# Optimization experiments

Hardware: AMD Instinct MI355X
Metric: run time of the kernel (lower is better)

## Reference

```python
import jax, jax.numpy as jnp
import numpy as np

NUM_EXPERTS = 8
HIDDEN = 2048
EXPERT_DIM = 4096
R = 64
LORA_ALPHA = 16
SCALING = LORA_ALPHA / R
TOKENS_PER_EXPERT = 1024


def setup_inputs() -> dict:
    key = jax.random.key(0)
    ks = jax.random.split(key, 7)
    s = lambda shape: 1.0 / np.sqrt(shape[-1])
    return {
        "hidden_states": jax.random.normal(ks[0], (NUM_EXPERTS * TOKENS_PER_EXPERT, HIDDEN), jnp.float32),
        "W_gu": jax.random.normal(ks[1], (2 * EXPERT_DIM, HIDDEN), jnp.float32) * s((HIDDEN,)),
        "A_gu": jax.random.normal(ks[2], (R, HIDDEN), jnp.float32) * s((HIDDEN,)),
        "B_gu": jax.random.normal(ks[3], (2 * EXPERT_DIM, R), jnp.float32) * 0.01,
        "W_d": jax.random.normal(ks[4], (HIDDEN, EXPERT_DIM), jnp.float32) * s((EXPERT_DIM,)),
        "A_d": jax.random.normal(ks[5], (R, EXPERT_DIM), jnp.float32) * s((EXPERT_DIM,)),
        "B_d": jax.random.normal(ks[6], (HIDDEN, R), jnp.float32) * 0.01,
    }


def _lora_linear(x, W, A, B):
    # y = x @ W^T + scaling * (x @ A^T) @ B^T   (nn.Linear convention, no dropout)
    return x @ W.T + (x @ A.T) @ B.T * SCALING


def reference(hidden_states, W_gu, A_gu, B_gu, W_d, A_d, B_d):
    # (E, N, H)
    x = hidden_states.reshape(NUM_EXPERTS, -1, HIDDEN)
    gate_up = _lora_linear(x, W_gu, A_gu, B_gu)          # (E, N, 2*D)
    gate, up = jnp.split(gate_up, 2, axis=-1)             # each (E, N, D)
    h = up * jax.nn.silu(gate)                            # SwiGLU
    out = _lora_linear(h, W_d, A_d, B_d)                  # (E, N, H)
    return out.reshape(-1, HIDDEN)
```

## Files before the change

### kernel.cpp

```cpp
#include <hip/hip_runtime.h>
#include <stdint.h>

typedef __bf16 bf16_t;
typedef __bf16 bf16x8 __attribute__((ext_vector_type(8)));
typedef __bf16 bf16x4 __attribute__((ext_vector_type(4)));
typedef float f32x4 __attribute__((ext_vector_type(4)));

#define GLOAD16(gp, lp)                                                        \
    __builtin_amdgcn_global_load_lds(                                          \
        (const __attribute__((address_space(1))) void*)(gp),                   \
        (__attribute__((address_space(3))) void*)(lp), 16, 0, 0)

#define MFMA16(a, b, c) __builtin_amdgcn_mfma_f32_16x16x32_bf16(a, b, c, 0, 0, 0)

#define SB() __builtin_amdgcn_sched_barrier(0)
#define BAR() asm volatile("s_barrier" ::: "memory")
#define LGKM0() asm volatile("s_waitcnt lgkmcnt(0)" ::: "memory")
#define VMW(n) asm volatile("s_waitcnt vmcnt(" #n ")" ::: "memory")

#define PHASE(GATE, STAGE, PF, MM)                                             \
    do {                                                                       \
        GATE;                                                                  \
        STAGE;                                                                 \
        SB();                                                                  \
        BAR();                                                                 \
        LGKM0();                                                               \
        SB();                                                                  \
        __builtin_amdgcn_s_setprio(1);                                         \
        PF;                                                                    \
        SB();                                                                  \
        MM;                                                                    \
        __builtin_amdgcn_s_setprio(0);                                         \
        SB();                                                                  \
        BAR();                                                                 \
    } while (0)

#define MMCL(aa, bb, mo, no)                                                   \
    do {                                                                       \
        _Pragma("unroll") for (int m_ = 0; m_ < 4; ++m_) {                     \
            _Pragma("unroll") for (int n_ = 0; n_ < 2; ++n_) {                 \
                acc[mo + m_][no + n_] =                                        \
                    MFMA16(aa[m_][0], bb[n_][0], acc[mo + m_][no + n_]);       \
                acc[mo + m_][no + n_] =                                        \
                    MFMA16(aa[m_][1], bb[n_][1], acc[mo + m_][no + n_]);       \
            }                                                                  \
        }                                                                      \
    } while (0)

#define PFA(dst, base, ro)                                                     \
    do {                                                                       \
        _Pragma("unroll") for (int m_ = 0; m_ < 4; ++m_) {                     \
            dst[m_][0] = *(const bf16x8*)((base) + offA0 + (ro + m_) * 1024);  \
            dst[m_][1] = *(const bf16x8*)((base) + offA1 + (ro + m_) * 1024);  \
        }                                                                      \
    } while (0)
#define PFB(dst, base, no)                                                     \
    do {                                                                       \
        _Pragma("unroll") for (int n_ = 0; n_ < 2; ++n_) {                     \
            dst[n_][0] = *(const bf16x8*)((base) + offB0 + (no + n_) * 1024);  \
            dst[n_][1] = *(const bf16x8*)((base) + offB1 + (no + n_) * 1024);  \
        }                                                                      \
    } while (0)


__global__ __launch_bounds__(256) void cvt_all_kernel(
    const float* __restrict__ x, const float* __restrict__ Wgu,
    const float* __restrict__ Bgu, const float* __restrict__ Wd,
    const float* __restrict__ Bd, const float* __restrict__ Agu,
    const float* __restrict__ Ad, bf16_t* __restrict__ X1,
    bf16_t* __restrict__ W1, bf16_t* __restrict__ W2,
    bf16_t* __restrict__ Abf, bf16_t* __restrict__ Adbf) {
    int b = blockIdx.x;
    const float* src;
    bf16_t* dst;
    int cshift, cmask, ldd, coff, lb;
    if (b < 16384) {
        src = x; dst = X1; cshift = 11; cmask = 2047; ldd = 2112; coff = 0; lb = b;
    } else if (b < 32768) {
        src = Wgu; dst = W1; cshift = 11; cmask = 2047; ldd = 2112; coff = 0; lb = b - 16384;
    } else if (b < 33280) {
        src = Bgu; dst = W1; cshift = 6; cmask = 63; ldd = 2112; coff = 2048; lb = b - 32768;
    } else if (b < 41472) {
        src = Wd; dst = W2; cshift = 12; cmask = 4095; ldd = 4160; coff = 0; lb = b - 33280;
    } else if (b < 41600) {
        src = Bd; dst = W2; cshift = 6; cmask = 63; ldd = 4160; coff = 4096; lb = b - 41472;
    } else if (b < 41728) {
        src = Agu; dst = Abf; cshift = 11; cmask = 2047; ldd = 2048; coff = 0; lb = b - 41600;
    } else {
        src = Ad; dst = Adbf; cshift = 12; cmask = 4095; ldd = 4096; coff = 0; lb = b - 41728;
    }
    int idx = (lb * 256 + threadIdx.x) << 2;
    int r = idx >> cshift;
    int c = idx & cmask;
    float4 v = *(const float4*)(src + idx);
    bf16x4 o = {(bf16_t)v.x, (bf16_t)v.y, (bf16_t)v.z, (bf16_t)v.w};
    *(bf16x4*)(dst + (size_t)r * ldd + coff + c) = o;
}

__global__ __launch_bounds__(256) void lora_kernel(const bf16_t* __restrict__ A,
                                                   int lda,
                                                   const bf16_t* __restrict__ Bw,
                                                   int K, bf16_t* __restrict__ dst,
                                                   int ldd, int coff) {
    __shared__ __align__(16) bf16_t As[64 * 64];
    __shared__ __align__(16) bf16_t Bs[64 * 64];
    const int t = threadIdx.x;
    const int m0 = blockIdx.x * 64;
    const int lane = t & 63, w = t >> 6;
    const int ln15 = lane & 15, q = lane >> 4;

    const int lrow = t >> 3;
    const int lchunk = (t & 7) ^ (lrow & 7);
    const bf16_t* gaL = A + (size_t)(m0 + lrow) * lda + lchunk * 8;
    const bf16_t* gbL = Bw + (size_t)lrow * K + lchunk * 8;
    bf16_t* lA = As + t * 8;
    bf16_t* lB = Bs + t * 8;

    const f32x4 z = {0.f, 0.f, 0.f, 0.f};
    f32x4 acc[4];
#pragma unroll
    for (int j = 0; j < 4; ++j) acc[j] = z;

    int aoffs[2], boffs[2][4];
#pragma unroll
    for (int s = 0; s < 2; ++s) {
        int rowa = w * 16 + ln15;
        aoffs[s] = rowa * 64 + (((q + 4 * s) ^ (rowa & 7)) << 3);
#pragma unroll
        for (int j = 0; j < 4; ++j) {
            int rowb = j * 16 + ln15;
            boffs[s][j] = rowb * 64 + (((q + 4 * s) ^ (rowb & 7)) << 3);
        }
    }

    for (int kt = 0; kt < K; kt += 64) {
        GLOAD16(gaL, lA);
        GLOAD16(gaL + (size_t)32 * lda, lA + 32 * 64);
        GLOAD16(gbL, lB);
        GLOAD16(gbL + (size_t)32 * K, lB + 32 * 64);
        __syncthreads();
#pragma unroll
        for (int s = 0; s < 2; ++s) {
            bf16x8 av = *(const bf16x8*)(As + aoffs[s]);
#pragma unroll
            for (int j = 0; j < 4; ++j) {
                bf16x8 bv = *(const bf16x8*)(Bs + boffs[s][j]);
                acc[j] = MFMA16(av, bv, acc[j]);
            }
        }
        __syncthreads();
        gaL += 64;
        gbL += 64;
    }

#pragma unroll
    for (int j = 0; j < 4; ++j)
#pragma unroll
        for (int rg = 0; rg < 4; ++rg) {
            int m = m0 + w * 16 + q * 4 + rg;
            dst[(size_t)m * ldd + coff + j * 16 + ln15] = (bf16_t)(acc[j][rg] * 0.25f);
        }
}

template <int LDA_, int LDB_, int NT_>
__device__ __forceinline__ void gemm8p_core(const bf16_t* __restrict__ gA,
                                            const bf16_t* __restrict__ gB0,
                                            const bf16_t* __restrict__ gB2,
                                            bf16_t* smem, const int t,
                                            const int offA0, const int offA1,
                                            const int offB0, const int offB1,
                                            f32x4 (&acc)[8][4]) {
    static_assert(NT_ & 1, "NT_ must be odd (pairs + tail tile)");
    bf16_t* const As0 = smem;
    bf16_t* const As1 = smem + 16384;
    bf16_t* const Bs0 = smem + 32768;
    bf16_t* const Bs1 = smem + 49152;

    auto stgA0 = [&](int kt, bf16_t* d) {
        GLOAD16(gA + kt, d + t * 8);
        GLOAD16(gA + (size_t)128 * LDA_ + kt, d + 128 * 64 + t * 8);
    };
    auto stgA1 = [&](int kt, bf16_t* d) {
        GLOAD16(gA + (size_t)64 * LDA_ + kt, d + 64 * 64 + t * 8);
        GLOAD16(gA + (size_t)192 * LDA_ + kt, d + 192 * 64 + t * 8);
    };
    auto stgBlo = [&](int kt, bf16_t* d) {
        GLOAD16(gB0 + kt, d + t * 8);
        GLOAD16(gB0 + (size_t)64 * LDB_ + kt, d + 64 * 64 + t * 8);
    };
    auto stgBhi = [&](int kt, bf16_t* d) {
        GLOAD16(gB2 + kt, d + 128 * 64 + t * 8);
        GLOAD16(gB2 + (size_t)64 * LDB_ + kt, d + 192 * 64 + t * 8);
    };

    bf16x8 a0[4][2], a1[4][2], b0e[2][2], b0o[2][2], b1v[2][2];

    stgA0(0, As0);
    stgA1(0, As0);
    stgBlo(0, Bs0);
    stgBhi(0, Bs0);
    stgA0(64, As1);
    stgBlo(64, Bs1);
    stgBhi(64, Bs1);
    VMW(6);
    BAR();
    PFA(a0, As0, 0);
    PFB(b0e, Bs0, 0);

    for (int g = 0; g + 2 < NT_; g += 2) {
        const int k1 = (g + 1) << 6, k2 = (g + 2) << 6, k3 = (g + 3) << 6;
        const bool s3 = (g + 3 < NT_);

        PHASE((void)0, stgA1(k1, As1), PFB(b1v, Bs0, 2), MMCL(a0, b0e, 0, 0));
        PHASE((void)0, stgA0(k2, As0), PFA(a1, As0, 4), MMCL(a0, b1v, 0, 2));
        PHASE(VMW(4), stgBlo(k2, Bs0), PFB(b0o, Bs1, 0), MMCL(a1, b1v, 4, 2));
        PHASE((void)0, stgBhi(k2, Bs0), PFA(a0, As1, 0), MMCL(a1, b0e, 4, 0));
        PHASE((void)0, stgA1(k2, As0), PFB(b1v, Bs1, 2), MMCL(a0, b0o, 0, 0));
        PHASE(VMW(8), if (s3) stgA0(k3, As1), PFA(a1, As1, 4),
              MMCL(a0, b1v, 0, 2));
        PHASE(VMW(2), if (s3) stgBlo(k3, Bs1), PFB(b0e, Bs0, 0),
              MMCL(a1, b1v, 4, 2));
        PHASE((void)0, if (s3) stgBhi(k3, Bs1), PFA(a0, As0, 0),
              MMCL(a1, b0o, 4, 0));
    }

    PHASE((void)0, (void)0, PFB(b1v, Bs0, 2), MMCL(a0, b0e, 0, 0));
    PHASE(VMW(0), (void)0, PFA(a1, As0, 4), MMCL(a0, b1v, 0, 2));
    PHASE((void)0, (void)0, (void)0, MMCL(a1, b1v, 4, 2));
    PHASE((void)0, (void)0, (void)0, MMCL(a1, b0e, 4, 0));
}

__device__ __forceinline__ int eswz(int row, int col) {
    return col ^ (((row >> 2) & 1) << 4) ^ (((row >> 3) & 3) << 2);
}

__global__ __launch_bounds__(512, 2) void gemm1_8p_kernel(
    const bf16_t* __restrict__ X, const bf16_t* __restrict__ Wc,
    bf16_t* __restrict__ X2) {
    __shared__ __align__(16) bf16_t smem[65536];
    const int t = threadIdx.x;
    const int lane = t & 63, wid = t >> 6;
    const int wr = wid >> 2, wc = wid & 3;
    const int ln15 = lane & 15, q = lane >> 4;
    const int n0 = blockIdx.x * 128;
    const int m0 = blockIdx.y * 256;

    const int sw = ln15 & 7;
    const int offA0 = (wr * 128 + ln15) * 64 + ((q ^ sw) << 3);
    const int offA1 = (wr * 128 + ln15) * 64 + (((q + 4) ^ sw) << 3);
    const int offB0 = (wc * 64 + ln15) * 64 + ((q ^ sw) << 3);
    const int offB1 = (wc * 64 + ln15) * 64 + (((q + 4) ^ sw) << 3);

    const int rr = t >> 3;
    const int lch = (t & 7) ^ (rr & 7);
    const bf16_t* gA = X + (size_t)(m0 + rr) * 2112 + lch * 8;
    const bf16_t* gB0 = Wc + (size_t)(n0 + rr) * 2112 + lch * 8;
    const bf16_t* gB2 = Wc + (size_t)(4096 + n0 + rr) * 2112 + lch * 8;

    f32x4 acc[8][4];
    const f32x4 z = {0.f, 0.f, 0.f, 0.f};
#pragma unroll
    for (int i = 0; i < 8; ++i)
#pragma unroll
        for (int j = 0; j < 4; ++j) acc[i][j] = z;

    gemm8p_core<2112, 2112, 33>(gA, gB0, gB2, smem, t, offA0, offA1, offB0,
                                offB1, acc);

    __syncthreads();
    float* fs = (float*)smem;
    if (wc >= 2) {
#pragma unroll
        for (int mi = 0; mi < 8; ++mi)
#pragma unroll
            for (int nj = 0; nj < 4; ++nj)
#pragma unroll
                for (int rg = 0; rg < 4; ++rg) {
                    int row = wr * 128 + mi * 16 + q * 4 + rg;
                    int col = (wc - 2) * 64 + nj * 16 + ln15;
                    fs[row * 128 + eswz(row, col)] = acc[mi][nj][rg];
                }
    }
    __syncthreads();
    if (wc < 2) {
#pragma unroll
        for (int mi = 0; mi < 8; ++mi)
#pragma unroll
            for (int nj = 0; nj < 4; ++nj)
#pragma unroll
                for (int rg = 0; rg < 4; ++rg) {
                    int row = wr * 128 + mi * 16 + q * 4 + rg;
                    int col = wc * 64 + nj * 16 + ln15;
                    float gv = acc[mi][nj][rg];
                    float uv = fs[row * 128 + eswz(row, col)];
                    float h = uv * gv / (1.f + __expf(-gv));
                    X2[(size_t)(m0 + row) * 4160 + (n0 + col)] = (bf16_t)h;
                }
    }
}

__global__ __launch_bounds__(512, 2) void gemm2_8p_kernel(
    const bf16_t* __restrict__ X2, const bf16_t* __restrict__ Wdc,
    float* __restrict__ out) {
    __shared__ __align__(16) bf16_t smem[65536];
    const int t = threadIdx.x;
    const int lane = t & 63, wid = t >> 6;
    const int wr = wid >> 2, wc = wid & 3;
    const int ln15 = lane & 15, q = lane >> 4;
    const int n0 = blockIdx.x * 256;
    const int m0 = blockIdx.y * 256;

    const int sw = ln15 & 7;
    const int offA0 = (wr * 128 + ln15) * 64 + ((q ^ sw) << 3);
    const int offA1 = (wr * 128 + ln15) * 64 + (((q + 4) ^ sw) << 3);
    const int offB0 = (wc * 64 + ln15) * 64 + ((q ^ sw) << 3);
    const int offB1 = (wc * 64 + ln15) * 64 + (((q + 4) ^ sw) << 3);

    const int rr = t >> 3;
    const int lch = (t & 7) ^ (rr & 7);
    const bf16_t* gA = X2 + (size_t)(m0 + rr) * 4160 + lch * 8;
    const bf16_t* gB0 = Wdc + (size_t)(n0 + rr) * 4160 + lch * 8;
    const bf16_t* gB2 = Wdc + (size_t)(n0 + 128 + rr) * 4160 + lch * 8;

    f32x4 acc[8][4];
    const f32x4 z = {0.f, 0.f, 0.f, 0.f};
#pragma unroll
    for (int i = 0; i < 8; ++i)
#pragma unroll
        for (int j = 0; j < 4; ++j) acc[i][j] = z;

    gemm8p_core<4160, 4160, 65>(gA, gB0, gB2, smem, t, offA0, offA1, offB0,
                                offB1, acc);

#pragma unroll
    for (int mi = 0; mi < 8; ++mi)
#pragma unroll
        for (int nj = 0; nj < 4; ++nj)
#pragma unroll
            for (int rg = 0; rg < 4; ++rg) {
                int row = wr * 128 + mi * 16 + q * 4 + rg;
                int col = wc * 64 + nj * 16 + ln15;
                out[(size_t)(m0 + row) * 2048 + (n0 + col)] = acc[mi][nj][rg];
            }
}

extern "C" void kernel_launch(void* const* d_in, const int* in_sizes, int n_in,
                              void* d_out, int out_size, void* d_ws, size_t ws_size,
                              hipStream_t stream) {
    const float* x = (const float*)d_in[0];
    const float* Wgu = (const float*)d_in[1];
    const float* Agu = (const float*)d_in[2];
    const float* Bgu = (const float*)d_in[3];
    const float* Wd = (const float*)d_in[4];
    const float* Ad = (const float*)d_in[5];
    const float* Bd = (const float*)d_in[6];
    float* out = (float*)d_out;

    char* ws = (char*)d_ws;
    bf16_t* X1 = (bf16_t*)(ws);
    bf16_t* W1 = (bf16_t*)(ws + 34603008);
    bf16_t* X2 = (bf16_t*)(ws + 69206016);
    bf16_t* W2 = (bf16_t*)(ws + 137363456);
    bf16_t* Abf = (bf16_t*)(ws + 154402816);
    bf16_t* Adbf = (bf16_t*)(ws + 154664960);

    cvt_all_kernel<<<41984, 256, 0, stream>>>(x, Wgu, Bgu, Wd, Bd, Agu, Ad,
                                              X1, W1, W2, Abf, Adbf);

    lora_kernel<<<128, 256, 0, stream>>>(X1, 2112, Abf, 2048, X1, 2112, 2048);
    gemm1_8p_kernel<<<dim3(32, 32), 512, 0, stream>>>(X1, W1, X2);
    lora_kernel<<<128, 256, 0, stream>>>(X2, 4160, Adbf, 4096, X2, 4160, 4096);
    gemm2_8p_kernel<<<dim3(8, 32), 512, 0, stream>>>(X2, W2, out);
}
```

Measured before the change: 662.8 us.

## Replace 8-phase GEMM pipeline with 4-phase per-k-tile double-buffered schedule

Restructures the shared GEMM core from an 8-phase schedule that spans two k-tiles into a simpler 4-phase loop per k-tile, alternating between two shared-memory buffers. Each phase loads A/B fragments for one k-half and issues 16 MFMAs while the next tile's global-to-LDS copies are staged. Loads past the last tile are clamped to the final tile instead of being skipped. The aim is simpler code with fewer fragment registers, but the new schedule runs more barriers per MFMA and may expose LDS reads before compute, so load-compute overlap could get worse.

```diff
diff --git a/kernel.cpp b/kernel.cpp
--- a/kernel.cpp
+++ b/kernel.cpp
@@ -18,47 +18,28 @@
 #define LGKM0() asm volatile("s_waitcnt lgkmcnt(0)" ::: "memory")
 #define VMW(n) asm volatile("s_waitcnt vmcnt(" #n ")" ::: "memory")
 
-#define PHASE(GATE, STAGE, PF, MM)                                             \
+#define PH_PRE()                                                               \
     do {                                                                       \
-        GATE;                                                                  \
-        STAGE;                                                                 \
         SB();                                                                  \
         BAR();                                                                 \
         LGKM0();                                                               \
         SB();                                                                  \
         __builtin_amdgcn_s_setprio(1);                                         \
-        PF;                                                                    \
-        SB();                                                                  \
-        MM;                                                                    \
+    } while (0)
+#define PH_POST()                                                              \
+    do {                                                                       \
         __builtin_amdgcn_s_setprio(0);                                         \
         SB();                                                                  \
         BAR();                                                                 \
     } while (0)
 
-#define MMCL(aa, bb, mo, no)                                                   \
+#define CL16(aa, bb, mo)                                                       \
     do {                                                                       \
-        _Pragma("unroll") for (int m_ = 0; m_ < 4; ++m_) {                     \
-            _Pragma("unroll") for (int n_ = 0; n_ < 2; ++n_) {                 \
-                acc[mo + m_][no + n_] =                                        \
-                    MFMA16(aa[m_][0], bb[n_][0], acc[mo + m_][no + n_]);       \
-                acc[mo + m_][no + n_] =                                        \
-                    MFMA16(aa[m_][1], bb[n_][1], acc[mo + m_][no + n_]);       \
+        _Pragma("unroll") for (int mi_ = 0; mi_ < 4; ++mi_) {                  \
+            _Pragma("unroll") for (int nj_ = 0; nj_ < 4; ++nj_) {              \
+                acc[(mo) + mi_][nj_] =                                         \
+                    MFMA16(aa[mi_], bb[nj_], acc[(mo) + mi_][nj_]);            \
             }                                                                  \
-        }                                                                      \
-    } while (0)
-
-#define PFA(dst, base, ro)                                                     \
-    do {                                                                       \
-        _Pragma("unroll") for (int m_ = 0; m_ < 4; ++m_) {                     \
-            dst[m_][0] = *(const bf16x8*)((base) + offA0 + (ro + m_) * 1024);  \
-            dst[m_][1] = *(const bf16x8*)((base) + offA1 + (ro + m_) * 1024);  \
-        }                                                                      \
-    } while (0)
-#define PFB(dst, base, no)                                                     \
-    do {                                                                       \
-        _Pragma("unroll") for (int n_ = 0; n_ < 2; ++n_) {                     \
-            dst[n_][0] = *(const bf16x8*)((base) + offB0 + (no + n_) * 1024);  \
-            dst[n_][1] = *(const bf16x8*)((base) + offB1 + (no + n_) * 1024);  \
         }                                                                      \
     } while (0)
 
@@ -163,19 +144,14 @@
 }
 
 template <int LDA_, int LDB_, int NT_>
-__device__ __forceinline__ void gemm8p_core(const bf16_t* __restrict__ gA,
+__device__ __forceinline__ void gemm4p_core(const bf16_t* __restrict__ gA,
                                             const bf16_t* __restrict__ gB0,
                                             const bf16_t* __restrict__ gB2,
                                             bf16_t* smem, const int t,
                                             const int offA0, const int offA1,
                                             const int offB0, const int offB1,
                                             f32x4 (&acc)[8][4]) {
-    static_assert(NT_ & 1, "NT_ must be odd (pairs + tail tile)");
-    bf16_t* const As0 = smem;
-    bf16_t* const As1 = smem + 16384;
-    bf16_t* const Bs0 = smem + 32768;
-    bf16_t* const Bs1 = smem + 49152;
-
+    constexpr int KLAST = (NT_ - 1) * 64;
     auto stgA0 = [&](int kt, bf16_t* d) {
         GLOAD16(gA + kt, d + t * 8);
         GLOAD16(gA + (size_t)128 * LDA_ + kt, d + 128 * 64 + t * 8);
@@ -193,41 +169,61 @@
         GLOAD16(gB2 + (size_t)64 * LDB_ + kt, d + 192 * 64 + t * 8);
     };
 
-    bf16x8 a0[4][2], a1[4][2], b0e[2][2], b0o[2][2], b1v[2][2];
-
-    stgA0(0, As0);
-    stgA1(0, As0);
-    stgBlo(0, Bs0);
-    stgBhi(0, Bs0);
-    stgA0(64, As1);
-    stgBlo(64, Bs1);
-    stgBhi(64, Bs1);
-    VMW(6);
+    bf16x8 aL[4], aH[4], bv[4];
+
+    stgA0(0, smem);
+    stgBlo(0, smem + 32768);
+    stgBhi(0, smem + 32768);
+    stgA1(0, smem);
+    stgA0(64 < KLAST ? 64 : KLAST, smem + 16384);
+    VMW(4);
     BAR();
-    PFA(a0, As0, 0);
-    PFB(b0e, Bs0, 0);
-
-    for (int g = 0; g + 2 < NT_; g += 2) {
-        const int k1 = (g + 1) << 6, k2 = (g + 2) << 6, k3 = (g + 3) << 6;
-        const bool s3 = (g + 3 < NT_);
-
-        PHASE((void)0, stgA1(k1, As1), PFB(b1v, Bs0, 2), MMCL(a0, b0e, 0, 0));
-        PHASE((void)0, stgA0(k2, As0), PFA(a1, As0, 4), MMCL(a0, b1v, 0, 2));
-        PHASE(VMW(4), stgBlo(k2, Bs0), PFB(b0o, Bs1, 0), MMCL(a1, b1v, 4, 2));
-        PHASE((void)0, stgBhi(k2, Bs0), PFA(a0, As1, 0), MMCL(a1, b0e, 4, 0));
-        PHASE((void)0, stgA1(k2, As0), PFB(b1v, Bs1, 2), MMCL(a0, b0o, 0, 0));
-        PHASE(VMW(8), if (s3) stgA0(k3, As1), PFA(a1, As1, 4),
-              MMCL(a0, b1v, 0, 2));
-        PHASE(VMW(2), if (s3) stgBlo(k3, Bs1), PFB(b0e, Bs0, 0),
-              MMCL(a1, b1v, 4, 2));
-        PHASE((void)0, if (s3) stgBhi(k3, Bs1), PFA(a0, As0, 0),
-              MMCL(a1, b0o, 4, 0));
-    }
-
-    PHASE((void)0, (void)0, PFB(b1v, Bs0, 2), MMCL(a0, b0e, 0, 0));
-    PHASE(VMW(0), (void)0, PFA(a1, As0, 4), MMCL(a0, b1v, 0, 2));
-    PHASE((void)0, (void)0, (void)0, MMCL(a1, b1v, 4, 2));
-    PHASE((void)0, (void)0, (void)0, MMCL(a1, b0e, 4, 0));
+
+    for (int g = 0; g < NT_; ++g) {
+        bf16_t* const Asc = smem + ((g & 1) << 14);
+        bf16_t* const Bsc = Asc + 32768;
+        bf16_t* const Asn = smem + (((g & 1) ^ 1) << 14);
+        bf16_t* const Bsn = Asn + 32768;
+        int k1 = (g + 1) << 6;
+        if (k1 > KLAST) k1 = KLAST;
+        int k2 = (g + 2) << 6;
+        if (k2 > KLAST) k2 = KLAST;
+
+#pragma unroll
+        for (int i = 0; i < 4; ++i) aL[i] = *(const bf16x8*)(Asc + offA0 + i * 1024);
+#pragma unroll
+        for (int j = 0; j < 4; ++j) bv[j] = *(const bf16x8*)(Bsc + offB0 + j * 1024);
+        stgBlo(k1, Bsn);
+        VMW(4);
+        PH_PRE();
+        CL16(aL, bv, 0);
+        PH_POST();
+
+#pragma unroll
+        for (int i = 0; i < 4; ++i) aH[i] = *(const bf16x8*)(Asc + offA0 + (4 + i) * 1024);
+        stgBhi(k1, Bsn);
+        PH_PRE();
+        CL16(aH, bv, 4);
+        PH_POST();
+
+#pragma unroll
+        for (int i = 0; i < 4; ++i) aL[i] = *(const bf16x8*)(Asc + offA1 + i * 1024);
+#pragma unroll
+        for (int j = 0; j < 4; ++j) bv[j] = *(const bf16x8*)(Bsc + offB1 + j * 1024);
+        stgA1(k1, Asn);
+        PH_PRE();
+        CL16(aL, bv, 0);
+        PH_POST();
+
+#pragma unroll
+        for (int i = 0; i < 4; ++i) aH[i] = *(const bf16x8*)(Asc + offA1 + (4 + i) * 1024);
+        stgA0(k2, Asc);
+        VMW(4);
+        PH_PRE();
+        CL16(aH, bv, 4);
+        PH_POST();
+    }
+    VMW(0);
 }
 
 __device__ __forceinline__ int eswz(int row, int col) {
@@ -264,7 +260,7 @@
 #pragma unroll
         for (int j = 0; j < 4; ++j) acc[i][j] = z;
 
-    gemm8p_core<2112, 2112, 33>(gA, gB0, gB2, smem, t, offA0, offA1, offB0,
+    gemm4p_core<2112, 2112, 33>(gA, gB0, gB2, smem, t, offA0, offA1, offB0,
                                 offB1, acc);
 
     __syncthreads();
@@ -329,7 +325,7 @@
 #pragma unroll
         for (int j = 0; j < 4; ++j) acc[i][j] = z;
 
-    gemm8p_core<4160, 4160, 65>(gA, gB0, gB2, smem, t, offA0, offA1, offB0,
+    gemm4p_core<4160, 4160, 65>(gA, gB0, gB2, smem, t, offA0, offA1, offB0,
                                 offB1, acc);
 
 #pragma unroll
```

Measured after the change: 624.9 us. 5.7% less time.
